# Kernel tuning notes

Measured on AMD Instinct MI355X. Metric: run time of the kernel, lower is better.

Reference implementation:

```python
import jax, jax.numpy as jnp
import numpy as np
from jax import lax

VOCAB = 32000
EMBED = 300
HIDDEN = 1024
BATCH = 64
SEQLEN = 512


def setup_inputs() -> dict:
    key = jax.random.key(0)
    k1, k2, k3, k4 = jax.random.split(key, 4)
    seq = jax.random.randint(k1, (BATCH, SEQLEN), 0, VOCAB, dtype=jnp.int32)
    embedding_table = jax.random.normal(k2, (VOCAB, EMBED), dtype=jnp.float32) * 0.1
    # Keras LSTM params: kernel [E, 4H], recurrent_kernel [H, 4H], bias [4H]; gate order i,f,c,o
    kernel = jax.random.normal(k3, (EMBED, 4 * HIDDEN), dtype=jnp.float32) * (1.0 / np.sqrt(EMBED))
    recurrent_kernel = jax.random.normal(k4, (HIDDEN, 4 * HIDDEN), dtype=jnp.float32) * (1.0 / np.sqrt(HIDDEN))
    # Keras unit_forget_bias default: forget-gate bias = 1
    bias = jnp.concatenate([
        jnp.zeros((HIDDEN,), jnp.float32),
        jnp.ones((HIDDEN,), jnp.float32),
        jnp.zeros((2 * HIDDEN,), jnp.float32),
    ])
    return {"embedding_table": embedding_table, "kernel": kernel,
            "recurrent_kernel": recurrent_kernel, "bias": bias, "seq": seq}


def _masked_lstm(x, mask, kernel, recurrent_kernel, bias):
    # x: [B,T,E], mask: [B,T] bool. Returns final hidden state [B,H].
    B = x.shape[0]
    H = recurrent_kernel.shape[0]
    # precompute input projections for all steps: [T,B,4H]
    xz = jnp.einsum('bte,eg->tbg', x, kernel) + bias
    mask_t = mask.T  # [T,B]

    def step(carry, inp):
        h, c = carry
        zx, mt = inp  # zx [B,4H], mt [B]
        z = zx + h @ recurrent_kernel
        zi, zf, zg, zo = jnp.split(z, 4, axis=-1)
        i = jax.nn.sigmoid(zi)
        f = jax.nn.sigmoid(zf)
        g = jnp.tanh(zg)
        o = jax.nn.sigmoid(zo)
        c_new = f * c + i * g
        h_new = o * jnp.tanh(c_new)
        m = mt[:, None]
        h = jnp.where(m, h_new, h)
        c = jnp.where(m, c_new, c)
        return (h, c), None

    h0 = jnp.zeros((B, H), x.dtype)
    c0 = jnp.zeros((B, H), x.dtype)
    (h, _), _ = lax.scan(step, (h0, c0), (xz, mask_t))
    return h


def reference(embedding_table, kernel, recurrent_kernel, bias, seq):
    x = embedding_table[seq]          # [B,T,E] embedding lookup
    mask = seq != 0                   # mask_zero=True: token id 0 is padding
    return _masked_lstm(x, mask, kernel, recurrent_kernel, bias)
```

## Files before the change

kernel.cpp:

```cpp
#include <hip/hip_runtime.h>

#define TT 512
#define BB 64
#define EE 300
#define HH 1024
#define GG 4096
#define NSLOT 33

typedef _Float16 f16x8 __attribute__((ext_vector_type(8)));
typedef float f32x4 __attribute__((ext_vector_type(4)));


__device__ __forceinline__ float sigmf(float x) {
    return __fdividef(1.0f, 1.0f + __expf(-x));
}
__device__ __forceinline__ float tanhsf(float x) {
    float e = __expf(-2.0f * fabsf(x));
    float r = __fdividef(1.0f - e, 1.0f + e);
    return copysignf(r, x);
}

__global__ void mask_kernel(const int* __restrict__ seq, float* __restrict__ maskf) {
    int idx = blockIdx.x * 256 + threadIdx.x;
    int t = idx >> 6, b = idx & 63;
    maskf[idx] = (seq[b * TT + t] != 0) ? 1.0f : 0.0f;
}

__global__ __launch_bounds__(256)
void xgather_kernel(const float* __restrict__ emb, const int* __restrict__ seq,
                    _Float16* __restrict__ xA) {
    __shared__ float xrow[64 * 305];
    const int t = blockIdx.x, tid = threadIdx.x;
    const int r = tid >> 2, sub = tid & 3;
    const int row = seq[r * TT + t];
    for (int e = sub; e < EE; e += 4)
        xrow[r * 305 + e] = emb[row * EE + e];
    __syncthreads();
    unsigned int* dst = (unsigned int*)(xA + (size_t)t * 20480);
    for (int idx = tid; idx < 10240; idx += 256) {
        int el = idx << 1;
        int j = el & 7, b = (el >> 3) & 63, quad = (el >> 9) & 3, kb = el >> 11;
        int e = (kb << 5) + (quad << 3) + j;
        union { _Float16 h[2]; unsigned int u; } pk;
        pk.h[0] = (e < EE)     ? (_Float16)xrow[b * 305 + e]     : (_Float16)0.f;
        pk.h[1] = (e + 1 < EE) ? (_Float16)xrow[b * 305 + e + 1] : (_Float16)0.f;
        dst[idx] = pk.u;
    }
}

__global__ __launch_bounds__(512, 2)
void lstm_kernel(const _Float16* __restrict__ xA, const float* __restrict__ rk,
                 const float* __restrict__ wk, const float* __restrict__ bias,
                 const float* __restrict__ maskf, _Float16* __restrict__ hbuf,
                 unsigned int* __restrict__ flags, float* __restrict__ out) {
    __shared__ _Float16 RbL[16384];
    __shared__ _Float16 WbL[5120];
    __shared__ float zb[8704];
    __shared__ float cs[2048];
    __shared__ _Float16 hshh[256];
    const int tid = threadIdx.x;
    const int lane = tid & 63;
    const int w = tid >> 6;
    const int p = blockIdx.x;
    const int p4 = p << 2;
    const int cc = lane & 15, quad = lane >> 4;

    for (int i = tid; i < 16384; i += 512) {
        int k = i >> 4, c = i & 15;
        float v = rk[k * GG + ((c >> 2) << 10) + p4 + (c & 3)];
        RbL[((k >> 5) << 9) + (((k >> 3) & 3) << 7) + (c << 3) + (k & 7)] = (_Float16)v;
    }
    for (int i = tid; i < 5120; i += 512) {
        int e = i >> 4, c = i & 15;
        float v = (e < EE) ? wk[e * GG + ((c >> 2) << 10) + p4 + (c & 3)] : 0.f;
        WbL[((e >> 5) << 9) + (((e >> 3) & 3) << 7) + (c << 3) + (e & 7)] = (_Float16)v;
    }
    if (tid < 256) cs[tid] = 0.f;
    float bb[4];
    if (w < 4) {
#pragma unroll
        for (int gt = 0; gt < 4; ++gt)
            bb[gt] = bias[(gt << 10) + p4 + w];
    }
    int slot = 0, nslot = 1;
    float hown = 0.0f;
    const int fidx = (w << 5) + (lane & 31);
    const f16x8* RbH = (const f16x8*)RbL;
    const f16x8* WbH = (const f16x8*)WbL;
    __syncthreads();

    for (int t = 0; t < TT; ++t) {
        float m = maskf[(t << 6) + lane];
        f32x4 acc[4];
#pragma unroll
        for (int mt = 0; mt < 4; ++mt) acc[mt] = (f32x4){0.f, 0.f, 0.f, 0.f};

        const f16x8* xA8 = (const f16x8*)(xA + (size_t)t * 20480);
        {
            int kb = w;
            f16x8 bf = WbH[(kb << 6) + (quad << 4) + cc];
#pragma unroll
            for (int mt = 0; mt < 4; ++mt) {
                f16x8 af = xA8[(kb << 8) + (quad << 6) + (mt << 4) + cc];
                acc[mt] = __builtin_amdgcn_mfma_f32_16x16x32_f16(af, bf, acc[mt], 0, 0, 0);
            }
        }
        if (w < 2) {
            int kb = 8 + w;
            f16x8 bf = WbH[(kb << 6) + (quad << 4) + cc];
#pragma unroll
            for (int mt = 0; mt < 4; ++mt) {
                f16x8 af = xA8[(kb << 8) + (quad << 6) + (mt << 4) + cc];
                acc[mt] = __builtin_amdgcn_mfma_f32_16x16x32_f16(af, bf, acc[mt], 0, 0, 0);
            }
        }

        if (t > 0) {
            unsigned int tgt = (unsigned int)t;
            while (!__all((int)(__hip_atomic_load(flags + fidx, __ATOMIC_RELAXED,
                                                  __HIP_MEMORY_SCOPE_AGENT) >= tgt)))
                __builtin_amdgcn_s_sleep(1);
        }
        __builtin_amdgcn_sched_barrier(0);

        const f16x8* hA8 = (const f16x8*)(hbuf + (size_t)slot * 65536);
#pragma unroll
        for (int kc = 0; kc < 4; ++kc) {
            int kb = (w << 2) + kc;
            f16x8 bf = RbH[(kb << 6) + (quad << 4) + cc];
#pragma unroll
            for (int mt = 0; mt < 4; ++mt) {
                f16x8 af = hA8[(kb << 8) + (quad << 6) + (mt << 4) + cc];
                acc[mt] = __builtin_amdgcn_mfma_f32_16x16x32_f16(af, bf, acc[mt], 0, 0, 0);
            }
        }
#pragma unroll
        for (int mt = 0; mt < 4; ++mt)
            *(f32x4*)(zb + ((w << 4) + cc) * 68 + (mt << 4) + (quad << 2)) = acc[mt];
        __syncthreads();
        if (w < 4) {
            float z[4];
#pragma unroll
            for (int gt = 0; gt < 4; ++gt) {
                int c = (gt << 2) + w;
                float s = bb[gt];
#pragma unroll
                for (int wp = 0; wp < 8; ++wp) s += zb[((wp << 4) + c) * 68 + lane];
                z[gt] = s;
            }
            float fi = sigmf(z[0]);
            float ff = sigmf(z[1]);
            float fg = tanhsf(z[2]);
            float fo = sigmf(z[3]);
            float co = cs[(w << 6) + lane];
            float cn = fmaf(ff, co, fi * fg);
            cn = fmaf(m, cn - co, co);
            cs[(w << 6) + lane] = cn;
            float hc = fo * tanhsf(cn);
            hown = fmaf(m, hc - hown, hown);
            hshh[(lane << 2) + w] = (_Float16)hown;
        }
        __syncthreads();
        if (tid < 64) {
            unsigned long long hv = ((const unsigned long long*)hshh)[lane];
            size_t el = (size_t)nslot * 65536 + ((size_t)(p >> 3) << 11) +
                        ((size_t)((p >> 1) & 3) << 9) + (lane << 3) + ((p & 1) << 2);
            __hip_atomic_store((unsigned long long*)(hbuf + el), hv,
                               __ATOMIC_RELAXED, __HIP_MEMORY_SCOPE_AGENT);
        }
        __syncthreads();
        if (tid == 0)
            __hip_atomic_store(flags + p, (unsigned int)(t + 1),
                               __ATOMIC_RELAXED, __HIP_MEMORY_SCOPE_AGENT);
        slot = nslot;
        nslot = (nslot + 1 == NSLOT) ? 0 : nslot + 1;
    }
    if (w < 4) zb[(w << 6) + lane] = hown;
    __syncthreads();
    if (tid < 64) {
        float4 v = make_float4(zb[tid], zb[64 + tid], zb[128 + tid], zb[192 + tid]);
        *(float4*)(out + tid * HH + p4) = v;
    }
}

extern "C" void kernel_launch(void* const* d_in, const int* in_sizes, int n_in,
                              void* d_out, int out_size, void* d_ws, size_t ws_size,
                              hipStream_t stream) {
    const float* emb  = (const float*)d_in[0];
    const float* wk   = (const float*)d_in[1];
    const float* rk   = (const float*)d_in[2];
    const float* bias = (const float*)d_in[3];
    const int*   seq  = (const int*)d_in[4];
    float* out = (float*)d_out;
    char* ws = (char*)d_ws;

    const size_t off_hbuf = 1024;
    const size_t off_mask = off_hbuf + (size_t)NSLOT * 131072;
    const size_t off_xA   = off_mask + 131072;
    unsigned int* flags = (unsigned int*)ws;
    _Float16* hbuf  = (_Float16*)(ws + off_hbuf);
    float*    maskf = (float*)(ws + off_mask);
    _Float16* xA    = (_Float16*)(ws + off_xA);

    hipMemsetAsync(ws, 0, off_hbuf + 131072, stream);
    mask_kernel<<<128, 256, 0, stream>>>(seq, maskf);
    xgather_kernel<<<TT, 256, 0, stream>>>(emb, seq, xA);
    lstm_kernel<<<256, 512, 0, stream>>>(xA, rk, wk, bias, maskf, hbuf, flags, out);
}
```

Baseline: 1.880 ms.

## Remove per-step block barriers by double-buffering gate scratch and per-wave publishing

Double-buffers the shared gate-partial buffer by timestep parity so the next step's MFMA writes can't clobber data still being read. This lets the kernel drop two of the three __syncthreads per step. Each gate wave now publishes its own fp16 hidden value directly to global memory and bumps a shared counter, and the last wave sets the block's ready flag. Cell state moves from shared memory into registers. This shortens the serial per-step critical path of the recurrence, but relies on per-wave ordering (vmcnt wait plus an LDS atomic) to keep flag publication correct and issues narrower 16-bit stores.

Measured after the change: 3.994 ms. 2.12x slower.

```diff
diff --git a/kernel.cpp b/kernel.cpp
--- a/kernel.cpp
+++ b/kernel.cpp
@@ -55,9 +55,8 @@
                  unsigned int* __restrict__ flags, float* __restrict__ out) {
     __shared__ _Float16 RbL[16384];
     __shared__ _Float16 WbL[5120];
-    __shared__ float zb[8704];
-    __shared__ float cs[2048];
-    __shared__ _Float16 hshh[256];
+    __shared__ float zb[2][8704];
+    __shared__ unsigned int cnt;
     const int tid = threadIdx.x;
     const int lane = tid & 63;
     const int w = tid >> 6;
@@ -75,22 +74,23 @@
         float v = (e < EE) ? wk[e * GG + ((c >> 2) << 10) + p4 + (c & 3)] : 0.f;
         WbL[((e >> 5) << 9) + (((e >> 3) & 3) << 7) + (c << 3) + (e & 7)] = (_Float16)v;
     }
-    if (tid < 256) cs[tid] = 0.f;
-    float bb[4];
+    if (tid == 0) cnt = 0u;
+    float bb[4], c_st = 0.f, hown = 0.f;
     if (w < 4) {
 #pragma unroll
         for (int gt = 0; gt < 4; ++gt)
             bb[gt] = bias[(gt << 10) + p4 + w];
     }
     int slot = 0, nslot = 1;
-    float hown = 0.0f;
     const int fidx = (w << 5) + (lane & 31);
+    const size_t pub_off = ((size_t)(p >> 3) << 11) + ((size_t)((p >> 1) & 3) << 9)
+                           + ((size_t)lane << 3) + ((size_t)(p & 1) << 2) + (size_t)w;
     const f16x8* RbH = (const f16x8*)RbL;
     const f16x8* WbH = (const f16x8*)WbL;
     __syncthreads();
 
     for (int t = 0; t < TT; ++t) {
-        float m = maskf[(t << 6) + lane];
+        float m = (w < 4) ? maskf[(t << 6) + lane] : 0.f;
         f32x4 acc[4];
 #pragma unroll
         for (int mt = 0; mt < 4; ++mt) acc[mt] = (f32x4){0.f, 0.f, 0.f, 0.f};
@@ -134,10 +134,12 @@
                 acc[mt] = __builtin_amdgcn_mfma_f32_16x16x32_f16(af, bf, acc[mt], 0, 0, 0);
             }
         }
+        float* zbP = &zb[t & 1][0];
 #pragma unroll
         for (int mt = 0; mt < 4; ++mt)
-            *(f32x4*)(zb + ((w << 4) + cc) * 68 + (mt << 4) + (quad << 2)) = acc[mt];
+            *(f32x4*)(zbP + ((w << 4) + cc) * 68 + (mt << 4) + (quad << 2)) = acc[mt];
         __syncthreads();
+
         if (w < 4) {
             float z[4];
 #pragma unroll
@@ -145,42 +147,34 @@
                 int c = (gt << 2) + w;
                 float s = bb[gt];
 #pragma unroll
-                for (int wp = 0; wp < 8; ++wp) s += zb[((wp << 4) + c) * 68 + lane];
+                for (int wp = 0; wp < 8; ++wp) s += zbP[((wp << 4) + c) * 68 + lane];
                 z[gt] = s;
             }
             float fi = sigmf(z[0]);
             float ff = sigmf(z[1]);
             float fg = tanhsf(z[2]);
             float fo = sigmf(z[3]);
-            float co = cs[(w << 6) + lane];
-            float cn = fmaf(ff, co, fi * fg);
-            cn = fmaf(m, cn - co, co);
-            cs[(w << 6) + lane] = cn;
+            float cn = fmaf(ff, c_st, fi * fg);
+            cn = fmaf(m, cn - c_st, c_st);
+            c_st = cn;
             float hc = fo * tanhsf(cn);
             hown = fmaf(m, hc - hown, hown);
-            hshh[(lane << 2) + w] = (_Float16)hown;
-        }
-        __syncthreads();
-        if (tid < 64) {
-            unsigned long long hv = ((const unsigned long long*)hshh)[lane];
-            size_t el = (size_t)nslot * 65536 + ((size_t)(p >> 3) << 11) +
-                        ((size_t)((p >> 1) & 3) << 9) + (lane << 3) + ((p & 1) << 2);
-            __hip_atomic_store((unsigned long long*)(hbuf + el), hv,
-                               __ATOMIC_RELAXED, __HIP_MEMORY_SCOPE_AGENT);
-        }
-        __syncthreads();
-        if (tid == 0)
-            __hip_atomic_store(flags + p, (unsigned int)(t + 1),
-                               __ATOMIC_RELAXED, __HIP_MEMORY_SCOPE_AGENT);
+            union { _Float16 h; unsigned short u; } cv;
+            cv.h = (_Float16)hown;
+            __hip_atomic_store((unsigned short*)(hbuf + (size_t)nslot * 65536 + pub_off),
+                               cv.u, __ATOMIC_RELAXED, __HIP_MEMORY_SCOPE_AGENT);
+            __asm__ volatile("s_waitcnt vmcnt(0)" ::: "memory");
+            if (lane == 0) {
+                unsigned int old = atomicAdd(&cnt, 1u);
+                if (old == (unsigned int)((t << 2) + 3))
+                    __hip_atomic_store(flags + p, (unsigned int)(t + 1),
+                                       __ATOMIC_RELAXED, __HIP_MEMORY_SCOPE_AGENT);
+            }
+        }
         slot = nslot;
         nslot = (nslot + 1 == NSLOT) ? 0 : nslot + 1;
     }
-    if (w < 4) zb[(w << 6) + lane] = hown;
-    __syncthreads();
-    if (tid < 64) {
-        float4 v = make_float4(zb[tid], zb[64 + tid], zb[128 + tid], zb[192 + tid]);
-        *(float4*)(out + tid * HH + p4) = v;
-    }
+    if (w < 4) out[lane * HH + p4 + w] = hown;
 }
 
 extern "C" void kernel_launch(void* const* d_in, const int* in_sizes, int n_in,
```
